# Kernel tuning notes

Hardware: AMD Instinct MI355X
Metric: run time of the kernel (lower is better)

## Reference

```python
import jax, jax.numpy as jnp
import numpy as np

NUM_BANDS = 24
HID = 128
B = 8
T = 800
L = 192000


def _hann(K):
    # torch.hann_window default is periodic
    n = np.arange(K)
    return 0.5 * (1.0 - np.cos(2.0 * np.pi * n / K))


def _make_filter_bank(num_bands=NUM_BANDS, K=31):
    half = K // 2
    d = (np.arange(K) - half).astype(np.float64)
    ds = np.where(d == 0, 1.0, d)
    win = _hann(K)
    W = np.zeros((num_bands, 1, K), np.float64)
    for i in range(num_bands):
        cf = 100.0 + i * 7000.0 / num_bands
        w = np.where(d == 0, 1.0, np.sin(2.0 * np.pi * cf * ds / 24000.0) / (np.pi * ds + 1e-8))
        w = w * win
        w = w / (np.abs(w).sum() + 1e-8)
        W[i, 0] = w
    return jnp.asarray(W, jnp.float32)


def _make_noise_type_filters(K=63):
    half = K // 2
    d = (np.arange(K) - half).astype(np.float64)
    ds = np.where(d == 0, 1.0, d)
    win = _hann(K)
    f0 = np.where(d == 0, 1.0, -0.85 * np.sin(np.pi * ds / K) / (np.pi * ds + 1e-8))
    f1 = np.where(d == 0, 1.0, np.sin(np.pi * ds / (K / 2)) / (np.pi * ds + 1e-8) * np.exp(-np.abs(ds) / 5.0))
    f2 = np.sin(np.pi * d / (K * 2)) / np.maximum(1.0, np.pi * d)
    f3 = np.sin(np.pi * d / (K / 4)) / np.maximum(1.0, np.pi * d) * np.exp(-np.abs(d) / 10.0)
    F = np.stack([f0, f1, f2, f3], 0)
    F = F * win[None, :]
    F = F / (np.abs(F).sum(axis=1, keepdims=True) + 1e-8)
    return jnp.asarray(F[:, None, :], jnp.float32)  # [4,1,K]


def conv1d(x, w, pad):
    # x: [B,Cin,L], w: [Cout,Cin,K]; cross-correlation like torch Conv1d
    return jax.lax.conv_general_dilated(x, w, (1,), [(pad, pad)],
                                        dimension_numbers=('NCH', 'OIH', 'NCH'))


def linterp(x, L_out):
    # F.interpolate(mode='linear', align_corners=False) over last axis
    T_in = x.shape[-1]
    pos = (jnp.arange(L_out, dtype=x.dtype) + 0.5) * (T_in / L_out) - 0.5
    pos = jnp.clip(pos, 0.0, T_in - 1)
    i0 = jnp.floor(pos).astype(jnp.int32)
    i1 = jnp.minimum(i0 + 1, T_in - 1)
    w = pos - i0
    return jnp.take(x, i0, axis=-1) * (1.0 - w) + jnp.take(x, i1, axis=-1) * w


def _noise_gate(intensity, attack_rate):
    # intensity, attack_rate: [B,L]; audio_length > 4 always here
    diff = jnp.pad(intensity[:, 1:] - intensity[:, :-1], ((0, 0), (1, 0)))
    attack_mask = (diff > 0.1).astype(intensity.dtype)
    enhanced = jnp.clip(intensity + attack_mask * attack_rate * 0.3, 0.0, 1.0)
    inc = (diff > 0).astype(intensity.dtype)
    gate = intensity * (1.0 - inc) + enhanced * inc
    g = jnp.pad(gate, ((0, 0), (2, 2)), mode='reflect')[:, None, :]
    k = jnp.ones((1, 1, 5), gate.dtype) / 5.0
    return conv1d(g, k, 0)[:, 0, :]


def setup_inputs() -> dict:
    key = jax.random.key(0)
    ks = jax.random.split(key, 8)
    s = 0.05
    inp = {
        'condition': jax.random.normal(ks[0], (B, HID, T), jnp.float32),
        'white_noise': jax.random.normal(ks[1], (B, 1, L), jnp.float32),
        'np_w1': jax.random.normal(ks[2], (256, HID, 3), jnp.float32) * s,
        'np_b1': jnp.zeros((256,), jnp.float32),
        'np_w2': jax.random.normal(ks[3], (256, 256, 3), jnp.float32) * s,
        'np_b2': jnp.zeros((256,), jnp.float32),
        'np_w3': jax.random.normal(ks[4], (NUM_BANDS + 3, 256, 1), jnp.float32) * s,
        'np_b3': jnp.zeros((NUM_BANDS + 3,), jnp.float32),
        'ss_w1': jax.random.normal(ks[5], (128, HID, 3), jnp.float32) * s,
        'ss_b1': jnp.zeros((128,), jnp.float32),
        'ss_w2': jax.random.normal(ks[6], (4, 128, 1), jnp.float32) * s,
        'ss_b2': jnp.zeros((4,), jnp.float32),
        'fb_w': _make_filter_bank(),
        'nt_w': _make_noise_type_filters(),
        'audio_length': L,
    }
    return inp


def reference(condition, white_noise, np_w1, np_b1, np_w2, np_b2, np_w3, np_b3,
              ss_w1, ss_b1, ss_w2, ss_b2, fb_w, nt_w, audio_length):
    # noise predictor
    h = jax.nn.leaky_relu(conv1d(condition, np_w1, 1) + np_b1[None, :, None], 0.1)
    h = jax.nn.leaky_relu(conv1d(h, np_w2, 1) + np_b2[None, :, None], 0.1)
    noise_params = conv1d(h, np_w3, 0) + np_b3[None, :, None]  # [B,27,T]
    band_amps = jax.nn.sigmoid(noise_params[:, :NUM_BANDS])
    attack = jax.nn.sigmoid(noise_params[:, -3]) * 10.0
    release = jax.nn.sigmoid(noise_params[:, -2]) * 5.0  # computed but unused (as in source)
    intensity = jax.nn.sigmoid(noise_params[:, -1])
    # spectral shaper
    g = jax.nn.leaky_relu(conv1d(condition, ss_w1, 1) + ss_b1[None, :, None], 0.1)
    ntw = jax.nn.softmax(conv1d(g, ss_w2, 0) + ss_b2[None, :, None], axis=1)  # [B,4,T]
    # upsample frame-rate controls to sample rate
    band_up = linterp(band_amps, audio_length)   # [B,24,L]
    ntw_up = linterp(ntw, audio_length)          # [B,4,L]
    inten_up = linterp(intensity, audio_length)  # [B,L]
    attack_up = linterp(attack, audio_length)
    _release_up = linterp(release, audio_length)
    # noise-type filter bank (4 filters stacked as one conv)
    ftypes = conv1d(white_noise, nt_w, 31)                       # [B,4,L]
    filtered = jnp.sum(ftypes * ntw_up, axis=1, keepdims=True)   # [B,1,L]
    # 24-band filter bank stacked as one conv
    bands = conv1d(filtered, fb_w, 15)                           # [B,24,L]
    shaped = jnp.sum(bands * band_up, axis=1)                    # [B,L]
    gate = _noise_gate(inten_up, attack_up)
    return shaped * gate, gate
```

## Files before the change

kernel.cpp:

```cpp
#include <hip/hip_runtime.h>
#include <math.h>

static constexpr int B  = 8;
static constexpr int T  = 800;
static constexpr int L  = 192000;
static constexpr int NB = 24;
static constexpr float SCALE = 800.0f / 192000.0f;

typedef __bf16 bf8 __attribute__((ext_vector_type(8)));
typedef float  f4  __attribute__((ext_vector_type(4)));

__device__ __forceinline__ float sigf(float x) { return 1.0f / (1.0f + __expf(-x)); }
__device__ __forceinline__ float leaky(float x) { return x >= 0.0f ? x : 0.1f * x; }
__device__ __forceinline__ unsigned short f2bf(float f) {
    unsigned u = __float_as_uint(f);
    u = u + 0x7FFFu + ((u >> 16) & 1u);
    return (unsigned short)(u >> 16);
}
__device__ __forceinline__ float bflo(unsigned u) { return __uint_as_float(u << 16); }
__device__ __forceinline__ float bfhi(unsigned u) { return __uint_as_float(u & 0xffff0000u); }

__device__ __forceinline__ void interp_idx(int l, int& i0, int& i1, float& w) {
    float pos = ((float)l + 0.5f) * SCALE - 0.5f;
    pos = fminf(fmaxf(pos, 0.0f), (float)(T - 1));
    i0 = (int)pos;
    i1 = min(i0 + 1, T - 1);
    w = pos - (float)i0;
}

__global__ __launch_bounds__(256) void k_twm(const float* __restrict__ w1,
                                             const float* __restrict__ w2,
                                             const float* __restrict__ wss,
                                             unsigned short* __restrict__ wT1,
                                             unsigned short* __restrict__ wT2,
                                             unsigned short* __restrict__ wTs) {
    int idx = blockIdx.x * 256 + threadIdx.x;
    if (idx < 98304) {
        int tap = idx / (256 * 128), r = idx % (256 * 128);
        int cout = r / 128, cin = r % 128;
        wT1[idx] = f2bf(w1[(cout * 128 + cin) * 3 + tap]);
    } else if (idx < 98304 + 196608) {
        int j = idx - 98304;
        int tap = j / (256 * 256), r = j % (256 * 256);
        int cout = r / 256, cin = r % 256;
        wT2[j] = f2bf(w2[(cout * 256 + cin) * 3 + tap]);
    } else if (idx < 98304 + 196608 + 49152) {
        int j = idx - 294912;
        int tap = j / (128 * 128), r = j % (128 * 128);
        int cout = r / 128, cin = r % 128;
        wTs[j] = f2bf(wss[(cout * 128 + cin) * 3 + tap]);
    }
}

template<int CIN, int COUT, bool INBF>
__global__ __launch_bounds__(256) void k_conv3m(const void* __restrict__ xin,
                                                const unsigned short* __restrict__ wT,
                                                const float* __restrict__ bias,
                                                unsigned short* __restrict__ y) {
    constexpr int CINP = CIN + 8;
    constexpr int MT = COUT / 64;
    __shared__ unsigned short xs[18 * CINP];
    const int b = blockIdx.y;
    const int t0 = blockIdx.x * 16;
    const int tid = threadIdx.x;
    const float* xf = (const float*)xin;
    const unsigned short* xb = (const unsigned short*)xin;
    for (int i = tid; i < 18 * CIN; i += 256) {
        int cin = i / 18, tr = i % 18;
        int t = t0 + tr - 1;
        unsigned short bits = 0;
        if (t >= 0 && t < T) {
            if (INBF) bits = xb[(b * CIN + cin) * T + t];
            else      bits = f2bf(xf[(b * CIN + cin) * T + t]);
        }
        xs[tr * CINP + cin] = bits;
    }
    __syncthreads();
    const int wave = tid >> 6, lane = tid & 63;
    const int coutb = wave * (COUT / 4);
    const int nfr = lane & 15;
    const int ko8 = (lane >> 4) * 8;
    f4 acc[MT] = {};
#pragma unroll
    for (int tap = 0; tap < 3; ++tap) {
        const unsigned short* wp = wT + ((tap * COUT + coutb + nfr) * CIN + ko8);
        const unsigned short* xp = xs + (nfr + tap) * CINP + ko8;
#pragma unroll 2
        for (int kc = 0; kc < CIN; kc += 32) {
            bf8 bv = *reinterpret_cast<const bf8*>(xp + kc);
#pragma unroll
            for (int m = 0; m < MT; ++m) {
                bf8 av = *reinterpret_cast<const bf8*>(wp + m * 16 * CIN + kc);
                acc[m] = __builtin_amdgcn_mfma_f32_16x16x32_bf16(av, bv, acc[m], 0, 0, 0);
            }
        }
    }
    const int rb = (lane >> 4) * 4;
    const int tcol = lane & 15;
#pragma unroll
    for (int m = 0; m < MT; ++m) {
#pragma unroll
        for (int r = 0; r < 4; ++r) {
            int cout = coutb + m * 16 + rb + r;
            float v = leaky(acc[m][r] + bias[cout]);
            y[(b * COUT + cout) * T + t0 + tcol] = f2bf(v);
        }
    }
}

__global__ __launch_bounds__(256) void k_np_fused(const unsigned short* __restrict__ h1,
                                                  const unsigned short* __restrict__ wT,
                                                  const float* __restrict__ bias,
                                                  const float* __restrict__ w3,
                                                  const float* __restrict__ b3,
                                                  const float* __restrict__ fbw,
                                                  float* __restrict__ h_all,
                                                  float* __restrict__ attack,
                                                  float* __restrict__ inten) {
    constexpr int CIN = 256, COUT = 256, CINP = 264;
    __shared__ unsigned short xs[18 * CINP];
    __shared__ unsigned short h2s[16 * CINP];
    __shared__ float bnd[16][25];
    const int b = blockIdx.y;
    const int t0 = blockIdx.x * 16;
    const int tid = threadIdx.x;
    for (int i = tid; i < 18 * CIN; i += 256) {
        int cin = i / 18, tr = i % 18;
        int t = t0 + tr - 1;
        xs[tr * CINP + cin] = (t >= 0 && t < T) ? h1[(b * CIN + cin) * T + t]
                                                : (unsigned short)0;
    }
    __syncthreads();
    const int wave = tid >> 6, lane = tid & 63;
    const int coutb = wave * 64;
    const int nfr = lane & 15;
    const int ko8 = (lane >> 4) * 8;
    f4 acc[4] = {};
#pragma unroll
    for (int tap = 0; tap < 3; ++tap) {
        const unsigned short* wp = wT + ((tap * COUT + coutb + nfr) * CIN + ko8);
        const unsigned short* xp = xs + (nfr + tap) * CINP + ko8;
#pragma unroll 2
        for (int kc = 0; kc < CIN; kc += 32) {
            bf8 bv = *reinterpret_cast<const bf8*>(xp + kc);
#pragma unroll
            for (int m = 0; m < 4; ++m) {
                bf8 av = *reinterpret_cast<const bf8*>(wp + m * 16 * CIN + kc);
                acc[m] = __builtin_amdgcn_mfma_f32_16x16x32_bf16(av, bv, acc[m], 0, 0, 0);
            }
        }
    }
    const int rb = (lane >> 4) * 4;
    const int tcol = lane & 15;
#pragma unroll
    for (int m = 0; m < 4; ++m) {
        ushort4 pk;
        pk.x = f2bf(leaky(acc[m][0] + bias[coutb + m * 16 + rb + 0]));
        pk.y = f2bf(leaky(acc[m][1] + bias[coutb + m * 16 + rb + 1]));
        pk.z = f2bf(leaky(acc[m][2] + bias[coutb + m * 16 + rb + 2]));
        pk.w = f2bf(leaky(acc[m][3] + bias[coutb + m * 16 + rb + 3]));
        *reinterpret_cast<ushort4*>(&h2s[tcol * CINP + coutb + m * 16 + rb]) = pk;
    }
    __syncthreads();
    for (int i = tid; i < 27 * 16; i += 256) {
        int c = i >> 4, t = i & 15;
        float s = b3[c];
        const unsigned short* hp = &h2s[t * CINP];
        const float* wp3 = w3 + c * 256;
#pragma unroll 4
        for (int kk = 0; kk < 256; kk += 8) {
            uint4 u = *reinterpret_cast<const uint4*>(hp + kk);
            float4 wa = *reinterpret_cast<const float4*>(wp3 + kk);
            float4 wb = *reinterpret_cast<const float4*>(wp3 + kk + 4);
            s += bflo(u.x) * wa.x + bfhi(u.x) * wa.y
               + bflo(u.y) * wa.z + bfhi(u.y) * wa.w
               + bflo(u.z) * wb.x + bfhi(u.z) * wb.y
               + bflo(u.w) * wb.z + bfhi(u.w) * wb.w;
        }
        if (c < 24) bnd[t][c] = sigf(s);
        else if (c == 24) attack[b * T + t0 + t] = sigf(s) * 10.0f;
        else if (c == 26) inten[b * T + t0 + t] = sigf(s);
    }
    __syncthreads();
    for (int i = tid; i < 31 * 16; i += 256) {
        int k = i >> 4, t = i & 15;
        float s = 0.0f;
#pragma unroll
        for (int c = 0; c < NB; ++c) s += bnd[t][c] * fbw[c * 31 + k];
        h_all[(b * 31 + k) * T + t0 + t] = s;
    }
}

__global__ __launch_bounds__(256) void k_ss_fused(const float* __restrict__ cond,
                                                  const unsigned short* __restrict__ wT,
                                                  const float* __restrict__ bias,
                                                  const float* __restrict__ w2,
                                                  const float* __restrict__ b2,
                                                  const float* __restrict__ ntf,
                                                  float* __restrict__ g_all) {
    constexpr int CIN = 128, COUT = 128, CINP = 136;
    __shared__ unsigned short xs[18 * CINP];
    __shared__ unsigned short gs[16 * CINP];
    __shared__ float sv[16][5];
    __shared__ float nws[16][5];
    const int b = blockIdx.y;
    const int t0 = blockIdx.x * 16;
    const int tid = threadIdx.x;
    for (int i = tid; i < 18 * CIN; i += 256) {
        int cin = i / 18, tr = i % 18;
        int t = t0 + tr - 1;
        xs[tr * CINP + cin] = (t >= 0 && t < T) ? f2bf(cond[(b * CIN + cin) * T + t])
                                                : (unsigned short)0;
    }
    __syncthreads();
    const int wave = tid >> 6, lane = tid & 63;
    const int coutb = wave * 32;
    const int nfr = lane & 15;
    const int ko8 = (lane >> 4) * 8;
    f4 acc[2] = {};
#pragma unroll
    for (int tap = 0; tap < 3; ++tap) {
        const unsigned short* wp = wT + ((tap * COUT + coutb + nfr) * CIN + ko8);
        const unsigned short* xp = xs + (nfr + tap) * CINP + ko8;
#pragma unroll
        for (int kc = 0; kc < CIN; kc += 32) {
            bf8 bv = *reinterpret_cast<const bf8*>(xp + kc);
#pragma unroll
            for (int m = 0; m < 2; ++m) {
                bf8 av = *reinterpret_cast<const bf8*>(wp + m * 16 * CIN + kc);
                acc[m] = __builtin_amdgcn_mfma_f32_16x16x32_bf16(av, bv, acc[m], 0, 0, 0);
            }
        }
    }
    const int rb = (lane >> 4) * 4;
    const int tcol = lane & 15;
#pragma unroll
    for (int m = 0; m < 2; ++m) {
        ushort4 pk;
        pk.x = f2bf(leaky(acc[m][0] + bias[coutb + m * 16 + rb + 0]));
        pk.y = f2bf(leaky(acc[m][1] + bias[coutb + m * 16 + rb + 1]));
        pk.z = f2bf(leaky(acc[m][2] + bias[coutb + m * 16 + rb + 2]));
        pk.w = f2bf(leaky(acc[m][3] + bias[coutb + m * 16 + rb + 3]));
        *reinterpret_cast<ushort4*>(&gs[tcol * CINP + coutb + m * 16 + rb]) = pk;
    }
    __syncthreads();
    if (tid < 64) {
        int c = tid & 3, tl = tid >> 2;
        float s = b2[c];
#pragma unroll
        for (int kk = 0; kk < 128; kk += 8) {
            uint4 u = *reinterpret_cast<const uint4*>(&gs[tl * CINP + kk]);
            float4 wa = *reinterpret_cast<const float4*>(&w2[c * 128 + kk]);
            float4 wb = *reinterpret_cast<const float4*>(&w2[c * 128 + kk + 4]);
            s += bflo(u.x) * wa.x + bfhi(u.x) * wa.y
               + bflo(u.y) * wa.z + bfhi(u.y) * wa.w
               + bflo(u.z) * wb.x + bfhi(u.z) * wb.y
               + bflo(u.w) * wb.z + bfhi(u.w) * wb.w;
        }
        sv[tl][c] = s;
    }
    __syncthreads();
    if (tid < 16) {
        float a0 = sv[tid][0], a1 = sv[tid][1], a2 = sv[tid][2], a3 = sv[tid][3];
        float m = fmaxf(fmaxf(a0, a1), fmaxf(a2, a3));
        float e0 = __expf(a0 - m), e1 = __expf(a1 - m), e2 = __expf(a2 - m), e3 = __expf(a3 - m);
        float inv = 1.0f / (e0 + e1 + e2 + e3);
        nws[tid][0] = e0 * inv; nws[tid][1] = e1 * inv;
        nws[tid][2] = e2 * inv; nws[tid][3] = e3 * inv;
    }
    __syncthreads();
    for (int i = tid; i < 63 * 16; i += 256) {
        int k = i >> 4, t = i & 15;
        float s = nws[t][0] * ntf[k] + nws[t][1] * ntf[63 + k]
                + nws[t][2] * ntf[126 + k] + nws[t][3] * ntf[189 + k];
        g_all[(b * 63 + k) * T + t0 + t] = s;
    }
}

__device__ __forceinline__ float interp_T(const float* __restrict__ a, int b, int p) {
    int i0, i1; float w;
    interp_idx(p, i0, i1, w);
    return a[b * T + i0] * (1.0f - w) + a[b * T + i1] * w;
}

__device__ __forceinline__ int refl(int p) {
    return p < 0 ? -p : (p >= L ? 2 * L - 2 - p : p);
}

__global__ __launch_bounds__(256) void k_sr(const float* __restrict__ wn,
                                            const float* __restrict__ g_all,
                                            const float* __restrict__ h_all,
                                            const float* __restrict__ attack,
                                            const float* __restrict__ inten,
                                            float* __restrict__ out) {
    __shared__ float wns[348];
    __shared__ float gl[4][63];
    __shared__ float hl[4][31];
    __shared__ float flt[286];
    __shared__ float ipl[261];
    __shared__ float gp[260];
    const int b = blockIdx.y;
    const int l0 = blockIdx.x * 256;
    const int tid = threadIdx.x;
    for (int i = tid; i < 348; i += 256) {
        int p = l0 - 46 + i;
        wns[i] = (p >= 0 && p < L) ? wn[b * L + p] : 0.0f;
    }
    int fg0, fgu; float wgu;
    interp_idx(l0 - 15, fg0, fgu, wgu);
    for (int i = tid; i < 376; i += 256) {
        if (i < 252) {
            int j = i / 63, k = i % 63;
            int f = min(fg0 + j, T - 1);
            gl[j][k] = g_all[(b * 63 + k) * T + f];
        } else {
            int j2 = (i - 252) / 31, k2 = (i - 252) % 31;
            int f = min(fg0 + j2, T - 1);
            hl[j2][k2] = h_all[(b * 31 + k2) * T + f];
        }
    }
    for (int i = tid; i < 261; i += 256)
        ipl[i] = interp_T(inten, b, l0 - 3 + i);
    __syncthreads();
    for (int i = tid; i < 260; i += 256) {
        int p = l0 - 2 + i;
        int pr = refl(p);
        float cur = ipl[pr - l0 + 3];
        float prev = (pr == 0) ? cur : ipl[pr - 1 - l0 + 3];
        float diff = cur - prev;
        float ar = interp_T(attack, b, pr);
        float enh = fminf(fmaxf(cur + (diff > 0.1f ? ar * 0.3f : 0.0f), 0.0f), 1.0f);
        gp[i] = (diff > 0.0f) ? enh : cur;
    }
    for (int i = tid; i < 286; i += 256) {
        int p = l0 - 15 + i;
        float v = 0.0f;
        if (p >= 0 && p < L) {
            int i0, i1; float w;
            interp_idx(p, i0, i1, w);
            int d0 = min(max(i0 - fg0, 0), 3);
            int d1 = min(max(i1 - fg0, 0), 3);
            float a0 = 0.0f, a1 = 0.0f;
#pragma unroll
            for (int k = 0; k < 63; ++k) {
                float xk = wns[i + k];
                a0 += xk * gl[d0][k];
                a1 += xk * gl[d1][k];
            }
            v = (1.0f - w) * a0 + w * a1;
        }
        flt[i] = v;
    }
    __syncthreads();
    const int l = l0 + tid;
    int i0, i1; float w;
    interp_idx(l, i0, i1, w);
    int d0 = min(max(i0 - fg0, 0), 3);
    int d1 = min(max(i1 - fg0, 0), 3);
    float a0 = 0.0f, a1 = 0.0f;
#pragma unroll
    for (int k = 0; k < 31; ++k) {
        float xk = flt[tid + k];
        a0 += xk * hl[d0][k];
        a1 += xk * hl[d1][k];
    }
    float shaped = (1.0f - w) * a0 + w * a1;
    float g5 = (gp[tid] + gp[tid + 1] + gp[tid + 2] + gp[tid + 3] + gp[tid + 4]) * 0.2f;
    out[b * L + l] = shaped * g5;
    out[B * L + b * L + l] = g5;
}

extern "C" void kernel_launch(void* const* d_in, const int* in_sizes, int n_in,
                              void* d_out, int out_size, void* d_ws, size_t ws_size,
                              hipStream_t stream) {
    const float* cond  = (const float*)d_in[0];
    const float* wn    = (const float*)d_in[1];
    const float* np_w1 = (const float*)d_in[2];
    const float* np_b1 = (const float*)d_in[3];
    const float* np_w2 = (const float*)d_in[4];
    const float* np_b2 = (const float*)d_in[5];
    const float* np_w3 = (const float*)d_in[6];
    const float* np_b3 = (const float*)d_in[7];
    const float* ss_w1 = (const float*)d_in[8];
    const float* ss_b1 = (const float*)d_in[9];
    const float* ss_w2 = (const float*)d_in[10];
    const float* ss_b2 = (const float*)d_in[11];
    const float* fb_w  = (const float*)d_in[12];
    const float* nt_w  = (const float*)d_in[13];

    char* p = (char*)d_ws;
    unsigned short* wT1 = (unsigned short*)p; p += 196608;
    unsigned short* wT2 = (unsigned short*)p; p += 393216;
    unsigned short* wTs = (unsigned short*)p; p += 98304;
    unsigned short* h1  = (unsigned short*)p; p += 3276800;
    float* attack = (float*)p; p += 25600;
    float* inten  = (float*)p; p += 25600;
    float* g_all  = (float*)p; p += 1612800;
    float* h_all  = (float*)p; p += 793600;
    float* out = (float*)d_out;

    k_twm<<<1344, 256, 0, stream>>>(np_w1, np_w2, ss_w1, wT1, wT2, wTs);
    k_conv3m<128, 256, false><<<dim3(50, 8), 256, 0, stream>>>(cond, wT1, np_b1, h1);
    k_ss_fused<<<dim3(50, 8), 256, 0, stream>>>(cond, wTs, ss_b1, ss_w2, ss_b2, nt_w, g_all);
    k_np_fused<<<dim3(50, 8), 256, 0, stream>>>(h1, wT2, np_b2, np_w3, np_b3, fb_w,
                                                h_all, attack, inten);
    k_sr<<<dim3(750, 8), 256, 0, stream>>>(wn, g_all, h_all, attack, inten, out);
}
```

Baseline: 192.3 us.

## Fuse both conv stacks and spectral shaper into one mega kernel

Merges the first noise-param conv, the second conv plus heads, and the spectral-shaper path into one kernel, selected by blockIdx.z, so all three run in a single launch. The first conv is computed per tile with a halo (18 columns from 20 input rows) straight into shared memory, which removes the h1 global round-trip and two kernel launches. In exchange, it recomputes about 12% extra conv1 columns per tile. The shared-memory union also grows, which may lower occupancy.

```diff
diff --git a/kernel.cpp b/kernel.cpp
--- a/kernel.cpp
+++ b/kernel.cpp
@@ -52,228 +52,212 @@
     }
 }
 
-template<int CIN, int COUT, bool INBF>
-__global__ __launch_bounds__(256) void k_conv3m(const void* __restrict__ xin,
-                                                const unsigned short* __restrict__ wT,
-                                                const float* __restrict__ bias,
-                                                unsigned short* __restrict__ y) {
-    constexpr int CINP = CIN + 8;
-    constexpr int MT = COUT / 64;
-    __shared__ unsigned short xs[18 * CINP];
+union SMem {
+    struct {
+        unsigned short xs[20 * 136];
+        unsigned short h1s[18 * 264];
+        unsigned short h2s[16 * 264];
+        float bnd[16][25];
+    } np;
+    struct {
+        unsigned short xs[18 * 136];
+        unsigned short gs[16 * 136];
+        float sv[16][5];
+        float nws[16][5];
+    } ss;
+};
+
+__global__ __launch_bounds__(256) void k_mega(const float* __restrict__ cond,
+                                              const unsigned short* __restrict__ wT1,
+                                              const float* __restrict__ b1,
+                                              const unsigned short* __restrict__ wT2,
+                                              const float* __restrict__ b2np,
+                                              const float* __restrict__ w3,
+                                              const float* __restrict__ b3,
+                                              const float* __restrict__ fbw,
+                                              const unsigned short* __restrict__ wTs,
+                                              const float* __restrict__ bss,
+                                              const float* __restrict__ w2ss,
+                                              const float* __restrict__ b2ss,
+                                              const float* __restrict__ ntf,
+                                              float* __restrict__ h_all,
+                                              float* __restrict__ g_all,
+                                              float* __restrict__ attack,
+                                              float* __restrict__ inten) {
+    __shared__ SMem sm;
     const int b = blockIdx.y;
     const int t0 = blockIdx.x * 16;
     const int tid = threadIdx.x;
-    const float* xf = (const float*)xin;
-    const unsigned short* xb = (const unsigned short*)xin;
-    for (int i = tid; i < 18 * CIN; i += 256) {
-        int cin = i / 18, tr = i % 18;
-        int t = t0 + tr - 1;
-        unsigned short bits = 0;
-        if (t >= 0 && t < T) {
-            if (INBF) bits = xb[(b * CIN + cin) * T + t];
-            else      bits = f2bf(xf[(b * CIN + cin) * T + t]);
-        }
-        xs[tr * CINP + cin] = bits;
-    }
-    __syncthreads();
     const int wave = tid >> 6, lane = tid & 63;
-    const int coutb = wave * (COUT / 4);
     const int nfr = lane & 15;
     const int ko8 = (lane >> 4) * 8;
-    f4 acc[MT] = {};
-#pragma unroll
-    for (int tap = 0; tap < 3; ++tap) {
-        const unsigned short* wp = wT + ((tap * COUT + coutb + nfr) * CIN + ko8);
-        const unsigned short* xp = xs + (nfr + tap) * CINP + ko8;
-#pragma unroll 2
-        for (int kc = 0; kc < CIN; kc += 32) {
-            bf8 bv = *reinterpret_cast<const bf8*>(xp + kc);
-#pragma unroll
-            for (int m = 0; m < MT; ++m) {
-                bf8 av = *reinterpret_cast<const bf8*>(wp + m * 16 * CIN + kc);
-                acc[m] = __builtin_amdgcn_mfma_f32_16x16x32_bf16(av, bv, acc[m], 0, 0, 0);
-            }
-        }
-    }
     const int rb = (lane >> 4) * 4;
     const int tcol = lane & 15;
-#pragma unroll
-    for (int m = 0; m < MT; ++m) {
-#pragma unroll
-        for (int r = 0; r < 4; ++r) {
-            int cout = coutb + m * 16 + rb + r;
-            float v = leaky(acc[m][r] + bias[cout]);
-            y[(b * COUT + cout) * T + t0 + tcol] = f2bf(v);
-        }
-    }
-}
-
-__global__ __launch_bounds__(256) void k_np_fused(const unsigned short* __restrict__ h1,
-                                                  const unsigned short* __restrict__ wT,
-                                                  const float* __restrict__ bias,
-                                                  const float* __restrict__ w3,
-                                                  const float* __restrict__ b3,
-                                                  const float* __restrict__ fbw,
-                                                  float* __restrict__ h_all,
-                                                  float* __restrict__ attack,
-                                                  float* __restrict__ inten) {
-    constexpr int CIN = 256, COUT = 256, CINP = 264;
-    __shared__ unsigned short xs[18 * CINP];
-    __shared__ unsigned short h2s[16 * CINP];
-    __shared__ float bnd[16][25];
-    const int b = blockIdx.y;
-    const int t0 = blockIdx.x * 16;
-    const int tid = threadIdx.x;
-    for (int i = tid; i < 18 * CIN; i += 256) {
-        int cin = i / 18, tr = i % 18;
-        int t = t0 + tr - 1;
-        xs[tr * CINP + cin] = (t >= 0 && t < T) ? h1[(b * CIN + cin) * T + t]
-                                                : (unsigned short)0;
-    }
-    __syncthreads();
-    const int wave = tid >> 6, lane = tid & 63;
-    const int coutb = wave * 64;
-    const int nfr = lane & 15;
-    const int ko8 = (lane >> 4) * 8;
-    f4 acc[4] = {};
-#pragma unroll
-    for (int tap = 0; tap < 3; ++tap) {
-        const unsigned short* wp = wT + ((tap * COUT + coutb + nfr) * CIN + ko8);
-        const unsigned short* xp = xs + (nfr + tap) * CINP + ko8;
+
+    if (blockIdx.z == 0) {
+        for (int i = tid; i < 20 * 128; i += 256) {
+            int cin = i / 20, j = i % 20;
+            int t = t0 - 2 + j;
+            sm.np.xs[j * 136 + cin] = (t >= 0 && t < T) ? f2bf(cond[(b * 128 + cin) * T + t])
+                                                        : (unsigned short)0;
+        }
+        __syncthreads();
+        const int coutb = wave * 64;
+        f4 a1[2][4] = {};
+#pragma unroll
+        for (int tap = 0; tap < 3; ++tap) {
+#pragma unroll
+            for (int kc = 0; kc < 128; kc += 32) {
+                bf8 bv0 = *reinterpret_cast<const bf8*>(&sm.np.xs[(nfr + tap) * 136 + kc + ko8]);
+                bf8 bv1 = *reinterpret_cast<const bf8*>(&sm.np.xs[(nfr + 16 + tap) * 136 + kc + ko8]);
+#pragma unroll
+                for (int m = 0; m < 4; ++m) {
+                    bf8 av = *reinterpret_cast<const bf8*>(
+                        wT1 + ((tap * 256 + coutb + m * 16 + nfr) * 128 + kc + ko8));
+                    a1[0][m] = __builtin_amdgcn_mfma_f32_16x16x32_bf16(av, bv0, a1[0][m], 0, 0, 0);
+                    a1[1][m] = __builtin_amdgcn_mfma_f32_16x16x32_bf16(av, bv1, a1[1][m], 0, 0, 0);
+                }
+            }
+        }
+#pragma unroll
+        for (int nt = 0; nt < 2; ++nt) {
+            int lcol = nt * 16 + tcol;
+            if (lcol < 18) {
+                int gcol = t0 - 1 + lcol;
+                bool ok = (gcol >= 0 && gcol < T);
+#pragma unroll
+                for (int m = 0; m < 4; ++m) {
+                    ushort4 pk;
+                    if (ok) {
+                        pk.x = f2bf(leaky(a1[nt][m][0] + b1[coutb + m * 16 + rb + 0]));
+                        pk.y = f2bf(leaky(a1[nt][m][1] + b1[coutb + m * 16 + rb + 1]));
+                        pk.z = f2bf(leaky(a1[nt][m][2] + b1[coutb + m * 16 + rb + 2]));
+                        pk.w = f2bf(leaky(a1[nt][m][3] + b1[coutb + m * 16 + rb + 3]));
+                    } else {
+                        pk.x = pk.y = pk.z = pk.w = 0;
+                    }
+                    *reinterpret_cast<ushort4*>(&sm.np.h1s[lcol * 264 + coutb + m * 16 + rb]) = pk;
+                }
+            }
+        }
+        __syncthreads();
+        f4 a2[4] = {};
+#pragma unroll
+        for (int tap = 0; tap < 3; ++tap) {
 #pragma unroll 2
-        for (int kc = 0; kc < CIN; kc += 32) {
-            bf8 bv = *reinterpret_cast<const bf8*>(xp + kc);
-#pragma unroll
-            for (int m = 0; m < 4; ++m) {
-                bf8 av = *reinterpret_cast<const bf8*>(wp + m * 16 * CIN + kc);
-                acc[m] = __builtin_amdgcn_mfma_f32_16x16x32_bf16(av, bv, acc[m], 0, 0, 0);
-            }
-        }
-    }
-    const int rb = (lane >> 4) * 4;
-    const int tcol = lane & 15;
-#pragma unroll
-    for (int m = 0; m < 4; ++m) {
-        ushort4 pk;
-        pk.x = f2bf(leaky(acc[m][0] + bias[coutb + m * 16 + rb + 0]));
-        pk.y = f2bf(leaky(acc[m][1] + bias[coutb + m * 16 + rb + 1]));
-        pk.z = f2bf(leaky(acc[m][2] + bias[coutb + m * 16 + rb + 2]));
-        pk.w = f2bf(leaky(acc[m][3] + bias[coutb + m * 16 + rb + 3]));
-        *reinterpret_cast<ushort4*>(&h2s[tcol * CINP + coutb + m * 16 + rb]) = pk;
-    }
-    __syncthreads();
-    for (int i = tid; i < 27 * 16; i += 256) {
-        int c = i >> 4, t = i & 15;
-        float s = b3[c];
-        const unsigned short* hp = &h2s[t * CINP];
-        const float* wp3 = w3 + c * 256;
+            for (int kc = 0; kc < 256; kc += 32) {
+                bf8 bv = *reinterpret_cast<const bf8*>(&sm.np.h1s[(nfr + tap) * 264 + kc + ko8]);
+#pragma unroll
+                for (int m = 0; m < 4; ++m) {
+                    bf8 av = *reinterpret_cast<const bf8*>(
+                        wT2 + ((tap * 256 + coutb + m * 16 + nfr) * 256 + kc + ko8));
+                    a2[m] = __builtin_amdgcn_mfma_f32_16x16x32_bf16(av, bv, a2[m], 0, 0, 0);
+                }
+            }
+        }
+#pragma unroll
+        for (int m = 0; m < 4; ++m) {
+            ushort4 pk;
+            pk.x = f2bf(leaky(a2[m][0] + b2np[coutb + m * 16 + rb + 0]));
+            pk.y = f2bf(leaky(a2[m][1] + b2np[coutb + m * 16 + rb + 1]));
+            pk.z = f2bf(leaky(a2[m][2] + b2np[coutb + m * 16 + rb + 2]));
+            pk.w = f2bf(leaky(a2[m][3] + b2np[coutb + m * 16 + rb + 3]));
+            *reinterpret_cast<ushort4*>(&sm.np.h2s[tcol * 264 + coutb + m * 16 + rb]) = pk;
+        }
+        __syncthreads();
+        for (int i = tid; i < 27 * 16; i += 256) {
+            int c = i >> 4, t = i & 15;
+            float s = b3[c];
+            const unsigned short* hp = &sm.np.h2s[t * 264];
+            const float* wp3 = w3 + c * 256;
 #pragma unroll 4
-        for (int kk = 0; kk < 256; kk += 8) {
-            uint4 u = *reinterpret_cast<const uint4*>(hp + kk);
-            float4 wa = *reinterpret_cast<const float4*>(wp3 + kk);
-            float4 wb = *reinterpret_cast<const float4*>(wp3 + kk + 4);
-            s += bflo(u.x) * wa.x + bfhi(u.x) * wa.y
-               + bflo(u.y) * wa.z + bfhi(u.y) * wa.w
-               + bflo(u.z) * wb.x + bfhi(u.z) * wb.y
-               + bflo(u.w) * wb.z + bfhi(u.w) * wb.w;
-        }
-        if (c < 24) bnd[t][c] = sigf(s);
-        else if (c == 24) attack[b * T + t0 + t] = sigf(s) * 10.0f;
-        else if (c == 26) inten[b * T + t0 + t] = sigf(s);
-    }
-    __syncthreads();
-    for (int i = tid; i < 31 * 16; i += 256) {
-        int k = i >> 4, t = i & 15;
-        float s = 0.0f;
-#pragma unroll
-        for (int c = 0; c < NB; ++c) s += bnd[t][c] * fbw[c * 31 + k];
-        h_all[(b * 31 + k) * T + t0 + t] = s;
-    }
-}
-
-__global__ __launch_bounds__(256) void k_ss_fused(const float* __restrict__ cond,
-                                                  const unsigned short* __restrict__ wT,
-                                                  const float* __restrict__ bias,
-                                                  const float* __restrict__ w2,
-                                                  const float* __restrict__ b2,
-                                                  const float* __restrict__ ntf,
-                                                  float* __restrict__ g_all) {
-    constexpr int CIN = 128, COUT = 128, CINP = 136;
-    __shared__ unsigned short xs[18 * CINP];
-    __shared__ unsigned short gs[16 * CINP];
-    __shared__ float sv[16][5];
-    __shared__ float nws[16][5];
-    const int b = blockIdx.y;
-    const int t0 = blockIdx.x * 16;
-    const int tid = threadIdx.x;
-    for (int i = tid; i < 18 * CIN; i += 256) {
-        int cin = i / 18, tr = i % 18;
-        int t = t0 + tr - 1;
-        xs[tr * CINP + cin] = (t >= 0 && t < T) ? f2bf(cond[(b * CIN + cin) * T + t])
-                                                : (unsigned short)0;
-    }
-    __syncthreads();
-    const int wave = tid >> 6, lane = tid & 63;
-    const int coutb = wave * 32;
-    const int nfr = lane & 15;
-    const int ko8 = (lane >> 4) * 8;
-    f4 acc[2] = {};
-#pragma unroll
-    for (int tap = 0; tap < 3; ++tap) {
-        const unsigned short* wp = wT + ((tap * COUT + coutb + nfr) * CIN + ko8);
-        const unsigned short* xp = xs + (nfr + tap) * CINP + ko8;
-#pragma unroll
-        for (int kc = 0; kc < CIN; kc += 32) {
-            bf8 bv = *reinterpret_cast<const bf8*>(xp + kc);
-#pragma unroll
-            for (int m = 0; m < 2; ++m) {
-                bf8 av = *reinterpret_cast<const bf8*>(wp + m * 16 * CIN + kc);
-                acc[m] = __builtin_amdgcn_mfma_f32_16x16x32_bf16(av, bv, acc[m], 0, 0, 0);
-            }
-        }
-    }
-    const int rb = (lane >> 4) * 4;
-    const int tcol = lane & 15;
-#pragma unroll
-    for (int m = 0; m < 2; ++m) {
-        ushort4 pk;
-        pk.x = f2bf(leaky(acc[m][0] + bias[coutb + m * 16 + rb + 0]));
-        pk.y = f2bf(leaky(acc[m][1] + bias[coutb + m * 16 + rb + 1]));
-        pk.z = f2bf(leaky(acc[m][2] + bias[coutb + m * 16 + rb + 2]));
-        pk.w = f2bf(leaky(acc[m][3] + bias[coutb + m * 16 + rb + 3]));
-        *reinterpret_cast<ushort4*>(&gs[tcol * CINP + coutb + m * 16 + rb]) = pk;
-    }
-    __syncthreads();
-    if (tid < 64) {
-        int c = tid & 3, tl = tid >> 2;
-        float s = b2[c];
-#pragma unroll
-        for (int kk = 0; kk < 128; kk += 8) {
-            uint4 u = *reinterpret_cast<const uint4*>(&gs[tl * CINP + kk]);
-            float4 wa = *reinterpret_cast<const float4*>(&w2[c * 128 + kk]);
-            float4 wb = *reinterpret_cast<const float4*>(&w2[c * 128 + kk + 4]);
-            s += bflo(u.x) * wa.x + bfhi(u.x) * wa.y
-               + bflo(u.y) * wa.z + bfhi(u.y) * wa.w
-               + bflo(u.z) * wb.x + bfhi(u.z) * wb.y
-               + bflo(u.w) * wb.z + bfhi(u.w) * wb.w;
-        }
-        sv[tl][c] = s;
-    }
-    __syncthreads();
-    if (tid < 16) {
-        float a0 = sv[tid][0], a1 = sv[tid][1], a2 = sv[tid][2], a3 = sv[tid][3];
-        float m = fmaxf(fmaxf(a0, a1), fmaxf(a2, a3));
-        float e0 = __expf(a0 - m), e1 = __expf(a1 - m), e2 = __expf(a2 - m), e3 = __expf(a3 - m);
-        float inv = 1.0f / (e0 + e1 + e2 + e3);
-        nws[tid][0] = e0 * inv; nws[tid][1] = e1 * inv;
-        nws[tid][2] = e2 * inv; nws[tid][3] = e3 * inv;
-    }
-    __syncthreads();
-    for (int i = tid; i < 63 * 16; i += 256) {
-        int k = i >> 4, t = i & 15;
-        float s = nws[t][0] * ntf[k] + nws[t][1] * ntf[63 + k]
-                + nws[t][2] * ntf[126 + k] + nws[t][3] * ntf[189 + k];
-        g_all[(b * 63 + k) * T + t0 + t] = s;
+            for (int kk = 0; kk < 256; kk += 8) {
+                uint4 u = *reinterpret_cast<const uint4*>(hp + kk);
+                float4 wa = *reinterpret_cast<const float4*>(wp3 + kk);
+                float4 wb = *reinterpret_cast<const float4*>(wp3 + kk + 4);
+                s += bflo(u.x) * wa.x + bfhi(u.x) * wa.y
+                   + bflo(u.y) * wa.z + bfhi(u.y) * wa.w
+                   + bflo(u.z) * wb.x + bfhi(u.z) * wb.y
+                   + bflo(u.w) * wb.z + bfhi(u.w) * wb.w;
+            }
+            if (c < 24) sm.np.bnd[t][c] = sigf(s);
+            else if (c == 24) attack[b * T + t0 + t] = sigf(s) * 10.0f;
+            else if (c == 26) inten[b * T + t0 + t] = sigf(s);
+        }
+        __syncthreads();
+        for (int i = tid; i < 31 * 16; i += 256) {
+            int k = i >> 4, t = i & 15;
+            float s = 0.0f;
+#pragma unroll
+            for (int c = 0; c < NB; ++c) s += sm.np.bnd[t][c] * fbw[c * 31 + k];
+            h_all[(b * 31 + k) * T + t0 + t] = s;
+        }
+    } else {
+        for (int i = tid; i < 18 * 128; i += 256) {
+            int cin = i / 18, tr = i % 18;
+            int t = t0 + tr - 1;
+            sm.ss.xs[tr * 136 + cin] = (t >= 0 && t < T) ? f2bf(cond[(b * 128 + cin) * T + t])
+                                                         : (unsigned short)0;
+        }
+        __syncthreads();
+        const int coutb = wave * 32;
+        f4 acc[2] = {};
+#pragma unroll
+        for (int tap = 0; tap < 3; ++tap) {
+#pragma unroll
+            for (int kc = 0; kc < 128; kc += 32) {
+                bf8 bv = *reinterpret_cast<const bf8*>(&sm.ss.xs[(nfr + tap) * 136 + kc + ko8]);
+#pragma unroll
+                for (int m = 0; m < 2; ++m) {
+                    bf8 av = *reinterpret_cast<const bf8*>(
+                        wTs + ((tap * 128 + coutb + m * 16 + nfr) * 128 + kc + ko8));
+                    acc[m] = __builtin_amdgcn_mfma_f32_16x16x32_bf16(av, bv, acc[m], 0, 0, 0);
+                }
+            }
+        }
+#pragma unroll
+        for (int m = 0; m < 2; ++m) {
+            ushort4 pk;
+            pk.x = f2bf(leaky(acc[m][0] + bss[coutb + m * 16 + rb + 0]));
+            pk.y = f2bf(leaky(acc[m][1] + bss[coutb + m * 16 + rb + 1]));
+            pk.z = f2bf(leaky(acc[m][2] + bss[coutb + m * 16 + rb + 2]));
+            pk.w = f2bf(leaky(acc[m][3] + bss[coutb + m * 16 + rb + 3]));
+            *reinterpret_cast<ushort4*>(&sm.ss.gs[tcol * 136 + coutb + m * 16 + rb]) = pk;
+        }
+        __syncthreads();
+        if (tid < 64) {
+            int c = tid & 3, tl = tid >> 2;
+            float s = b2ss[c];
+#pragma unroll
+            for (int kk = 0; kk < 128; kk += 8) {
+                uint4 u = *reinterpret_cast<const uint4*>(&sm.ss.gs[tl * 136 + kk]);
+                float4 wa = *reinterpret_cast<const float4*>(&w2ss[c * 128 + kk]);
+                float4 wb = *reinterpret_cast<const float4*>(&w2ss[c * 128 + kk + 4]);
+                s += bflo(u.x) * wa.x + bfhi(u.x) * wa.y
+                   + bflo(u.y) * wa.z + bfhi(u.y) * wa.w
+                   + bflo(u.z) * wb.x + bfhi(u.z) * wb.y
+                   + bflo(u.w) * wb.z + bfhi(u.w) * wb.w;
+            }
+            sm.ss.sv[tl][c] = s;
+        }
+        __syncthreads();
+        if (tid < 16) {
+            float a0 = sm.ss.sv[tid][0], a1v = sm.ss.sv[tid][1];
+            float a2v = sm.ss.sv[tid][2], a3v = sm.ss.sv[tid][3];
+            float m = fmaxf(fmaxf(a0, a1v), fmaxf(a2v, a3v));
+            float e0 = __expf(a0 - m), e1 = __expf(a1v - m);
+            float e2 = __expf(a2v - m), e3 = __expf(a3v - m);
+            float inv = 1.0f / (e0 + e1 + e2 + e3);
+            sm.ss.nws[tid][0] = e0 * inv; sm.ss.nws[tid][1] = e1 * inv;
+            sm.ss.nws[tid][2] = e2 * inv; sm.ss.nws[tid][3] = e3 * inv;
+        }
+        __syncthreads();
+        for (int i = tid; i < 63 * 16; i += 256) {
+            int k = i >> 4, t = i & 15;
+            float s = sm.ss.nws[t][0] * ntf[k] + sm.ss.nws[t][1] * ntf[63 + k]
+                    + sm.ss.nws[t][2] * ntf[126 + k] + sm.ss.nws[t][3] * ntf[189 + k];
+            g_all[(b * 63 + k) * T + t0 + t] = s;
+        }
     }
 }
 
@@ -392,7 +376,6 @@
     unsigned short* wT1 = (unsigned short*)p; p += 196608;
     unsigned short* wT2 = (unsigned short*)p; p += 393216;
     unsigned short* wTs = (unsigned short*)p; p += 98304;
-    unsigned short* h1  = (unsigned short*)p; p += 3276800;
     float* attack = (float*)p; p += 25600;
     float* inten  = (float*)p; p += 25600;
     float* g_all  = (float*)p; p += 1612800;
@@ -400,9 +383,8 @@
     float* out = (float*)d_out;
 
     k_twm<<<1344, 256, 0, stream>>>(np_w1, np_w2, ss_w1, wT1, wT2, wTs);
-    k_conv3m<128, 256, false><<<dim3(50, 8), 256, 0, stream>>>(cond, wT1, np_b1, h1);
-    k_ss_fused<<<dim3(50, 8), 256, 0, stream>>>(cond, wTs, ss_b1, ss_w2, ss_b2, nt_w, g_all);
-    k_np_fused<<<dim3(50, 8), 256, 0, stream>>>(h1, wT2, np_b2, np_w3, np_b3, fb_w,
-                                                h_all, attack, inten);
+    k_mega<<<dim3(50, 8, 2), 256, 0, stream>>>(cond, wT1, np_b1, wT2, np_b2, np_w3, np_b3,
+                                               fb_w, wTs, ss_b1, ss_w2, ss_b2, nt_w,
+                                               h_all, g_all, attack, inten);
     k_sr<<<dim3(750, 8), 256, 0, stream>>>(wn, g_all, h_all, attack, inten, out);
 }
```

Result: faster. 176.4 us (-8.3%).
